# Performance work log

Measured on AMD Instinct MI355X. Metric: run time of the kernel, lower is better.

## Reference

```python
import jax, jax.numpy as jnp
import numpy as np

DIM = 512
HID = 512
H = 8
HD = HID // H
RB_HID = 64
COORD = 3


def setup_inputs() -> dict:
    key = jax.random.key(0)
    ks = jax.random.split(key, 12)
    B, Nq, Nk = 2, 1024, 2048
    s = 0.02
    return {
        "q_in": jax.random.normal(ks[0], (B, Nq, DIM), jnp.float32),
        "kv_in": jax.random.normal(ks[1], (B, Nk, DIM), jnp.float32),
        "q_coords": jax.random.normal(ks[2], (B, Nq, COORD), jnp.float32),
        "kv_coords": jax.random.normal(ks[3], (B, Nk, COORD), jnp.float32),
        "Wq": jax.random.normal(ks[4], (DIM, HID), jnp.float32) * s,
        "Wk": jax.random.normal(ks[5], (DIM, HID), jnp.float32) * s,
        "Wv": jax.random.normal(ks[6], (DIM, HID), jnp.float32) * s,
        "Wo": jax.random.normal(ks[7], (HID, DIM), jnp.float32) * s,
        "W1": jax.random.normal(ks[8], (1, RB_HID), jnp.float32) * s,
        "b1": jnp.zeros((RB_HID,), jnp.float32),
        "W2": jax.random.normal(ks[9], (RB_HID, H), jnp.float32) * s,
        "b2": jnp.zeros((H,), jnp.float32),
    }


def reference(q_in, kv_in, q_coords, kv_coords, Wq, Wk, Wv, Wo, W1, b1, W2, b2):
    B, Nq, _ = q_in.shape
    Nk = kv_in.shape[1]
    # projections -> [B, H, N, HD]
    q = (q_in @ Wq).reshape(B, Nq, H, HD).transpose(0, 2, 1, 3)
    k = (kv_in @ Wk).reshape(B, Nk, H, HD).transpose(0, 2, 1, 3)
    v = (kv_in @ Wv).reshape(B, Nk, H, HD).transpose(0, 2, 1, 3)
    # pairwise Euclidean distance [B, Nq, Nk]
    diff = q_coords[:, :, None, :] - kv_coords[:, None, :, :]
    d = jnp.sqrt(jnp.sum(diff * diff, axis=-1))
    # 2-layer MLP on distance -> per-head bias [B, H, Nq, Nk]
    h = jax.nn.silu(d[..., None] * W1[0] + b1)  # [B,Nq,Nk,RB_HID]
    bias = (h @ W2 + b2).transpose(0, 3, 1, 2)  # [B,H,Nq,Nk]
    scale = HD ** -0.5
    logits = jnp.einsum("bhqd,bhkd->bhqk", q, k) * scale + bias
    attn = jax.nn.softmax(logits, axis=-1)
    out = jnp.einsum("bhqk,bhkd->bhqd", attn, v)
    out = out.transpose(0, 2, 1, 3).reshape(B, Nq, HID)
    return out @ Wo
```

## Files before the change

kernel.cpp:

```cpp
#include <hip/hip_runtime.h>
#include <hip/hip_bf16.h>
#include <math.h>

typedef short bf16x8 __attribute__((ext_vector_type(8)));
typedef float f32x4 __attribute__((ext_vector_type(4)));
typedef unsigned short u16;
typedef unsigned int u32;

#define NH 8
#define BB 2
#define NQ 1024
#define NK 2048
#define NSPLIT 8
#define M2CONST 6.4921250
#define SC2 0.18033688f
#define LS 68

#define MFMA16(a, b, c) __builtin_amdgcn_mfma_f32_16x16x32_bf16(a, b, c, 0, 0, 0)

__device__ __constant__ double XN_D[6] = {251.63850576500074, 218.50966799187810,
                                          161.12883777312265, 94.871162226877350,
                                          37.490330081221910, 4.3614942349992570};

static __device__ __forceinline__ u32 bfr(float x) {
  u32 u = __builtin_bit_cast(u32, x);
  return u + 0x7FFFu + ((u >> 16) & 1u);
}
static __device__ __forceinline__ u32 pk2(float lo, float hi) {
  return (bfr(lo) >> 16) | (bfr(hi) & 0xFFFF0000u);
}
static __device__ __forceinline__ u16 bfs(float x) { return (u16)(bfr(x) >> 16); }

static __device__ __forceinline__ bf16x8 pack8(float4 a, float4 b) {
  union { bf16x8 v; uint4 u; } cv;
  cv.u.x = pk2(a.x, a.y);
  cv.u.y = pk2(a.z, a.w);
  cv.u.z = pk2(b.x, b.y);
  cv.u.w = pk2(b.z, b.w);
  return cv.v;
}

__global__ __launch_bounds__(256) void setup_kernel(
    const float* __restrict__ Wq, const float* __restrict__ Wk,
    const float* __restrict__ Wv, const float* __restrict__ Wo,
    u16* __restrict__ Tq, u16* __restrict__ Tk,
    u16* __restrict__ Tv, u16* __restrict__ To,
    const float* __restrict__ W1, const float* __restrict__ b1,
    const float* __restrict__ W2, const float* __restrict__ b2,
    float* __restrict__ polyc,
    const float* __restrict__ kc, u16* __restrict__ keg) {
  const int blk = blockIdx.x, t = threadIdx.x;
  if (blk < 256) {
    __shared__ u16 tile[64][65];
    const float* W; u16* Wt;
    switch (blk >> 6) {
      case 0: W = Wq; Wt = Tq; break;
      case 1: W = Wk; Wt = Tk; break;
      case 2: W = Wv; Wt = Tv; break;
      default: W = Wo; Wt = To; break;
    }
    const int rem = blk & 63;
    const int k0 = (rem >> 3) * 64, n0 = (rem & 7) * 64;
    const int r = t >> 4, c4 = (t & 15) * 4;
    #pragma unroll
    for (int p = 0; p < 4; p++) {
      int row = p * 16 + r;
      float4 v = *(const float4*)&W[(size_t)(k0 + row) * 512 + n0 + c4];
      tile[row][c4 + 0] = bfs(v.x);
      tile[row][c4 + 1] = bfs(v.y);
      tile[row][c4 + 2] = bfs(v.z);
      tile[row][c4 + 3] = bfs(v.w);
    }
    __syncthreads();
    #pragma unroll
    for (int p = 0; p < 4; p++) {
      int n = p * 16 + r;
      u16 u0 = tile[c4 + 0][n], u1 = tile[c4 + 1][n];
      u16 u2 = tile[c4 + 2][n], u3 = tile[c4 + 3][n];
      uint2 o;
      o.x = u0 | ((u32)u1 << 16);
      o.y = u2 | ((u32)u3 << 16);
      *(uint2*)&Wt[(size_t)(n0 + n) * 512 + k0 + c4] = o;
    }
  } else if (blk == 256) {
    __shared__ double fv[6][8];
    if (t < 48) {
      int i = t >> 3, h = t & 7;
      double x = sqrt(XN_D[i]);
      double acc = (double)b2[h];
      for (int r = 0; r < 64; r++) {
        double u = x * (double)W1[r] + (double)b1[r];
        double s = u / (1.0 + exp(-u));
        acc += s * (double)W2[r * 8 + h];
      }
      fv[i][h] = acc * 1.4426950408889634 - M2CONST;
    }
    __syncthreads();
    if (t < 8) {
      int h = t;
      double c[6];
      #pragma unroll
      for (int i = 0; i < 6; i++) c[i] = fv[i][h];
      for (int k = 1; k < 6; k++)
        for (int i = 5; i >= k; i--)
          c[i] = (c[i] - c[i - 1]) / (XN_D[i] - XN_D[i - k]);
      double m[6] = {c[5], 0, 0, 0, 0, 0};
      int deg = 0;
      for (int i = 4; i >= 0; i--) {
        double np[6] = {};
        for (int j = deg; j >= 0; j--) np[j + 1] += m[j];
        for (int j = 0; j <= deg; j++) np[j] -= XN_D[i] * m[j];
        np[0] += c[i];
        deg++;
        for (int j = 0; j <= deg; j++) m[j] = np[j];
      }
      #pragma unroll
      for (int j = 0; j < 6; j++) polyc[h * 8 + j] = (float)m[j];
    }
  } else {
    int r = (blk - 257) * 256 + t;
    float kx = kc[(size_t)r * 3], ky = kc[(size_t)r * 3 + 1], kz = kc[(size_t)r * 3 + 2];
    uint4 o;
    o.x = pk2(-2.0f * kx, -2.0f * ky);
    o.y = pk2(-2.0f * kz, 1.0f);
    o.z = (u32)bfs(kx * kx + ky * ky + kz * kz);
    o.w = 0;
    *(uint4*)&keg[(size_t)r * 8] = o;
  }
}

__global__ __launch_bounds__(256) void gemm_qkv(
    const float* __restrict__ q_in, const float* __restrict__ kv_in,
    const u16* __restrict__ Wqt, const u16* __restrict__ Wkt,
    const u16* __restrict__ Wvt, u16* __restrict__ Qp,
    u16* __restrict__ Kp, u16* __restrict__ Vtp) {
  __shared__ u16 As[64 * LS];
  __shared__ u16 Bs[64 * LS];
  __shared__ u16 Bs2[64 * LS];
  const int t = threadIdx.x;
  const int w = t >> 6, l = t & 63, g = l >> 4, li = l & 15;
  const int bx = blockIdx.x;
  const bool isQ = bx < 32;
  const int m0 = (isQ ? bx : bx - 32) * 64, n0 = blockIdx.y * 64;
  const float* A = isQ ? q_in : kv_in;
  const u16* B1 = isQ ? Wqt : Wkt;
  const int ms = (w & 1) * 32, ns = (w >> 1) * 32;
  const int ar = t >> 2, ac = (t & 3) * 16;
  f32x4 acc[2][2] = {}, accV[2][2] = {};

  for (int kt = 0; kt < 512; kt += 64) {
    float4 a4[4];
    #pragma unroll
    for (int q = 0; q < 4; q++)
      a4[q] = *(const float4*)&A[(size_t)(m0 + ar) * 512 + kt + ac + 4 * q];
    bf16x8 bk[2], bv2[2];
    #pragma unroll
    for (int p = 0; p < 2; p++) {
      int f = p * 256 + t, r = f >> 3, c8 = (f & 7) * 8;
      bk[p] = *(const bf16x8*)&B1[(size_t)(n0 + r) * 512 + kt + c8];
    }
    if (!isQ) {
      #pragma unroll
      for (int p = 0; p < 2; p++) {
        int f = p * 256 + t, r = f >> 3, c8 = (f & 7) * 8;
        bv2[p] = *(const bf16x8*)&Wvt[(size_t)(n0 + r) * 512 + kt + c8];
      }
    }
    __syncthreads();
    *(bf16x8*)&As[ar * LS + ac] = pack8(a4[0], a4[1]);
    *(bf16x8*)&As[ar * LS + ac + 8] = pack8(a4[2], a4[3]);
    #pragma unroll
    for (int p = 0; p < 2; p++) {
      int f = p * 256 + t, r = f >> 3, c8 = (f & 7) * 8;
      *(bf16x8*)&Bs[r * LS + c8] = bk[p];
    }
    if (!isQ) {
      #pragma unroll
      for (int p = 0; p < 2; p++) {
        int f = p * 256 + t, r = f >> 3, c8 = (f & 7) * 8;
        *(bf16x8*)&Bs2[r * LS + c8] = bv2[p];
      }
    }
    __syncthreads();
    #pragma unroll
    for (int ks = 0; ks < 2; ks++) {
      bf16x8 a0 = *(const bf16x8*)&As[(ms + li) * LS + ks * 32 + g * 8];
      bf16x8 a1 = *(const bf16x8*)&As[(ms + 16 + li) * LS + ks * 32 + g * 8];
      bf16x8 k0 = *(const bf16x8*)&Bs[(ns + li) * LS + ks * 32 + g * 8];
      bf16x8 k1 = *(const bf16x8*)&Bs[(ns + 16 + li) * LS + ks * 32 + g * 8];
      acc[0][0] = MFMA16(a0, k0, acc[0][0]);
      acc[0][1] = MFMA16(a0, k1, acc[0][1]);
      acc[1][0] = MFMA16(a1, k0, acc[1][0]);
      acc[1][1] = MFMA16(a1, k1, acc[1][1]);
      if (!isQ) {
        bf16x8 v0 = *(const bf16x8*)&Bs2[(ns + li) * LS + ks * 32 + g * 8];
        bf16x8 v1 = *(const bf16x8*)&Bs2[(ns + 16 + li) * LS + ks * 32 + g * 8];
        accV[0][0] = MFMA16(a0, v0, accV[0][0]);
        accV[0][1] = MFMA16(a0, v1, accV[0][1]);
        accV[1][0] = MFMA16(a1, v0, accV[1][0]);
        accV[1][1] = MFMA16(a1, v1, accV[1][1]);
      }
    }
  }
  #pragma unroll
  for (int mi = 0; mi < 2; mi++) {
    #pragma unroll
    for (int ni = 0; ni < 2; ni++) {
      int row = m0 + ms + mi * 16 + 4 * g;
      int col = n0 + ns + ni * 16 + li;
      f32x4 vk = acc[mi][ni];
      if (isQ) {
        #pragma unroll
        for (int r = 0; r < 4; r++) Qp[(size_t)(row + r) * 512 + col] = bfs(vk[r]);
      } else {
        #pragma unroll
        for (int r = 0; r < 4; r++) Kp[(size_t)(row + r) * 512 + col] = bfs(vk[r]);
        f32x4 vv = accV[mi][ni];
        int bb = row >> 11, j = row & 2047;
        int hh = col >> 6, d = col & 63;
        uint2 o;
        o.x = pk2(vv[0], vv[1]);
        o.y = pk2(vv[2], vv[3]);
        *(uint2*)&Vtp[((size_t)((bb * 8 + hh) * 64 + d)) * 2048 + j] = o;
      }
    }
  }
}

__global__ __launch_bounds__(256, 4) void attn_kernel(
    const u16* __restrict__ Qb, const u16* __restrict__ Kb,
    const u16* __restrict__ Vt, const float* __restrict__ qc,
    const u16* __restrict__ keg, const float* __restrict__ polyc,
    float* __restrict__ Op, float* __restrict__ Lp) {
  __shared__ u16 Kl[64 * LS];
  __shared__ u16 Vtl[64 * LS];
  __shared__ u16 Pl[64 * LS];

  const int t = threadIdx.x;
  const int w = t >> 6, l = t & 63, g = l >> 4, li = l & 15;
  const int qt = blockIdx.x >> 3, sidx = blockIdx.x & 7;
  const int h = blockIdx.y, b = blockIdx.z;

  const float c0 = polyc[h * 8 + 0], c1 = polyc[h * 8 + 1];
  const float c2 = polyc[h * 8 + 2], c3 = polyc[h * 8 + 3];
  const float c4 = polyc[h * 8 + 4], c5 = polyc[h * 8 + 5];

  const int qrow = qt * 64 + w * 16 + li;
  const size_t qg = (size_t)b * NQ + qrow;
  bf16x8 qf0 = *(const bf16x8*)&Qb[qg * 512 + h * 64 + g * 8];
  bf16x8 qf1 = *(const bf16x8*)&Qb[qg * 512 + h * 64 + 32 + g * 8];
  float qx = qc[qg * 3], qy = qc[qg * 3 + 1], qz = qc[qg * 3 + 2];
  bf16x8 qe = {};
  if (g == 0) {
    qe[0] = (short)bfs(qx);
    qe[1] = (short)bfs(qy);
    qe[2] = (short)bfs(qz);
    qe[3] = (short)bfs(qx * qx + qy * qy + qz * qz);
    qe[4] = (short)bfs(1.0f);
  }

  f32x4 oacc[4] = {};
  float lacc = 0.0f;

  const u16* Kg = Kb + (size_t)b * NK * 512 + h * 64;
  const u16* Vg = Vt + (size_t)((b * 8 + h) * 64) * 2048;
  const u16* keg_b = keg + (size_t)b * NK * 8;

  const int jb0 = sidx * (NK / NSPLIT);
  const int srow = t >> 3, sc8 = (t & 7) * 8;

  bf16x8 kr0 = *(const bf16x8*)&Kg[(size_t)(jb0 + srow) * 512 + sc8];
  bf16x8 kr1 = *(const bf16x8*)&Kg[(size_t)(jb0 + 32 + srow) * 512 + sc8];
  bf16x8 vr0 = *(const bf16x8*)&Vg[(size_t)srow * 2048 + jb0 + sc8];
  bf16x8 vr1 = *(const bf16x8*)&Vg[(size_t)(32 + srow) * 2048 + jb0 + sc8];

  for (int it = 0; it < NK / NSPLIT / 64; it++) {
    const int jbase = jb0 + it * 64;
    __syncthreads();
    *(bf16x8*)&Kl[srow * LS + sc8] = kr0;
    *(bf16x8*)&Kl[(32 + srow) * LS + sc8] = kr1;
    *(bf16x8*)&Vtl[srow * LS + sc8] = vr0;
    *(bf16x8*)&Vtl[(32 + srow) * LS + sc8] = vr1;
    __syncthreads();
    if (it + 1 < NK / NSPLIT / 64) {
      const int jn = jbase + 64;
      kr0 = *(const bf16x8*)&Kg[(size_t)(jn + srow) * 512 + sc8];
      kr1 = *(const bf16x8*)&Kg[(size_t)(jn + 32 + srow) * 512 + sc8];
      vr0 = *(const bf16x8*)&Vg[(size_t)srow * 2048 + jn + sc8];
      vr1 = *(const bf16x8*)&Vg[(size_t)(32 + srow) * 2048 + jn + sc8];
    }

    #pragma unroll
    for (int j4 = 0; j4 < 4; j4++) {
      bf16x8 ka0 = *(const bf16x8*)&Kl[(j4 * 16 + li) * LS + g * 8];
      bf16x8 ka1 = *(const bf16x8*)&Kl[(j4 * 16 + li) * LS + 32 + g * 8];
      f32x4 z = {};
      f32x4 s0 = MFMA16(ka0, qf0, z);
      f32x4 sac = MFMA16(ka1, qf1, s0);
      bf16x8 ke = {};
      if (g == 0)
        ke = *(const bf16x8*)&keg_b[(size_t)(jbase + j4 * 16 + li) * 8];
      f32x4 dac = MFMA16(ke, qe, z);

      float p[4];
      #pragma unroll
      for (int r = 0; r < 4; r++) {
        float u = fminf(dac[r], 256.0f);
        float gp = fmaf(fmaf(fmaf(fmaf(fmaf(c5, u, c4), u, c3), u, c2), u, c1), u, c0);
        p[r] = __builtin_amdgcn_exp2f(fmaf(sac[r], SC2, gp));
      }
      lacc += (p[0] + p[1]) + (p[2] + p[3]);
      uint2 pv;
      pv.x = pk2(p[0], p[1]);
      pv.y = pk2(p[2], p[3]);
      *(uint2*)&Pl[(w * 16 + li) * LS + j4 * 16 + g * 4] = pv;
    }

    bf16x8 pf0 = *(const bf16x8*)&Pl[(w * 16 + li) * LS + g * 8];
    bf16x8 pf1 = *(const bf16x8*)&Pl[(w * 16 + li) * LS + 32 + g * 8];
    #pragma unroll
    for (int dt = 0; dt < 4; dt++) {
      bf16x8 v0 = *(const bf16x8*)&Vtl[(dt * 16 + li) * LS + g * 8];
      bf16x8 v1 = *(const bf16x8*)&Vtl[(dt * 16 + li) * LS + 32 + g * 8];
      oacc[dt] = MFMA16(pf0, v0, oacc[dt]);
      oacc[dt] = MFMA16(pf1, v1, oacc[dt]);
    }
  }

  float lf = lacc;
  lf += __shfl_xor(lf, 16);
  lf += __shfl_xor(lf, 32);

  const size_t obase =
      ((size_t)(sidx * 16 + b * 8 + h) * 1024 + qt * 64 + w * 16) * 64;
  #pragma unroll
  for (int dt = 0; dt < 4; dt++)
    #pragma unroll
    for (int r = 0; r < 4; r++)
      Op[obase + (size_t)(4 * g + r) * 64 + dt * 16 + li] = oacc[dt][r];
  if (g == 0)
    Lp[(size_t)(sidx * 16 + b * 8 + h) * 1024 + qt * 64 + w * 16 + li] = lf;
}

__global__ __launch_bounds__(256) void combine_kernel(const float* __restrict__ Op,
                                                      const float* __restrict__ Lp,
                                                      u16* __restrict__ AOb) {
  int tid = blockIdx.x * 256 + threadIdx.x;
  int d4 = tid & 15, rh = tid >> 4;
  int bh = rh >> 10, qrow = rh & 1023;
  f32x4 o = {};
  float lsum = 0.0f;
  #pragma unroll
  for (int s = 0; s < NSPLIT; s++) {
    f32x4 v = *(const f32x4*)&Op[((size_t)(s * 16 + bh) * 1024 + qrow) * 64 + d4 * 4];
    o += v;
    lsum += Lp[(size_t)(s * 16 + bh) * 1024 + qrow];
  }
  float inv = __builtin_amdgcn_rcpf(lsum);
  uint2 pk;
  pk.x = pk2(o[0] * inv, o[1] * inv);
  pk.y = pk2(o[2] * inv, o[3] * inv);
  *(uint2*)&AOb[((size_t)(bh >> 3) * NQ + qrow) * 512 + (bh & 7) * 64 + d4 * 4] = pk;
}

__global__ __launch_bounds__(256) void gemm_wo(const u16* __restrict__ A,
                                               const u16* __restrict__ Bt,
                                               float* __restrict__ C) {
  __shared__ u16 As[32 * LS];
  __shared__ u16 Bs[64 * LS];
  const int t = threadIdx.x;
  const int w = t >> 6, l = t & 63, g = l >> 4, li = l & 15;
  const int m0 = blockIdx.x * 32, n0 = blockIdx.y * 64;
  const int ms = (w & 1) * 16, ns = (w >> 1) * 32;
  f32x4 acc[2] = {};
  for (int kt = 0; kt < 512; kt += 64) {
    bf16x8 av, bv[2];
    {
      int r = t >> 3, c8 = (t & 7) * 8;
      av = *(const bf16x8*)&A[(size_t)(m0 + r) * 512 + kt + c8];
    }
    #pragma unroll
    for (int p = 0; p < 2; p++) {
      int f = p * 256 + t, r = f >> 3, c8 = (f & 7) * 8;
      bv[p] = *(const bf16x8*)&Bt[(size_t)(n0 + r) * 512 + kt + c8];
    }
    __syncthreads();
    {
      int r = t >> 3, c8 = (t & 7) * 8;
      *(bf16x8*)&As[r * LS + c8] = av;
    }
    #pragma unroll
    for (int p = 0; p < 2; p++) {
      int f = p * 256 + t, r = f >> 3, c8 = (f & 7) * 8;
      *(bf16x8*)&Bs[r * LS + c8] = bv[p];
    }
    __syncthreads();
    #pragma unroll
    for (int ks = 0; ks < 2; ks++) {
      bf16x8 af = *(const bf16x8*)&As[(ms + li) * LS + ks * 32 + g * 8];
      bf16x8 b0 = *(const bf16x8*)&Bs[(ns + li) * LS + ks * 32 + g * 8];
      bf16x8 b1 = *(const bf16x8*)&Bs[(ns + 16 + li) * LS + ks * 32 + g * 8];
      acc[0] = MFMA16(af, b0, acc[0]);
      acc[1] = MFMA16(af, b1, acc[1]);
    }
  }
  #pragma unroll
  for (int ni = 0; ni < 2; ni++) {
    f32x4 v = acc[ni];
    int row = m0 + ms + 4 * g;
    int col = n0 + ns + ni * 16 + li;
    #pragma unroll
    for (int r = 0; r < 4; r++) C[(size_t)(row + r) * 512 + col] = v[r];
  }
}

extern "C" void kernel_launch(void* const* d_in, const int* in_sizes, int n_in,
                              void* d_out, int out_size, void* d_ws, size_t ws_size,
                              hipStream_t stream) {
  const float* q_in      = (const float*)d_in[0];
  const float* kv_in     = (const float*)d_in[1];
  const float* q_coords  = (const float*)d_in[2];
  const float* kv_coords = (const float*)d_in[3];
  const float* Wq        = (const float*)d_in[4];
  const float* Wk        = (const float*)d_in[5];
  const float* Wv        = (const float*)d_in[6];
  const float* Wo        = (const float*)d_in[7];
  const float* W1        = (const float*)d_in[8];
  const float* b1        = (const float*)d_in[9];
  const float* W2        = (const float*)d_in[10];
  const float* b2        = (const float*)d_in[11];

  char* p = (char*)d_ws;
  u16* Wqt  = (u16*)p; p += (size_t)512 * 512 * 2;
  u16* Wkt  = (u16*)p; p += (size_t)512 * 512 * 2;
  u16* Wvt  = (u16*)p; p += (size_t)512 * 512 * 2;
  u16* Wot  = (u16*)p; p += (size_t)512 * 512 * 2;
  u16* Qp   = (u16*)p; p += (size_t)2048 * 512 * 2;
  u16* Kp   = (u16*)p; p += (size_t)4096 * 512 * 2;
  u16* Vtp  = (u16*)p; p += (size_t)4096 * 512 * 2;
  u16* AOb  = (u16*)p; p += (size_t)2048 * 512 * 2;
  u16* keg  = (u16*)p; p += (size_t)4096 * 8 * 2;
  float* polyc = (float*)p; p += (size_t)64 * 4;
  p = (char*)(((size_t)p + 255) & ~(size_t)255);
  float* Opart = (float*)p; p += (size_t)NSPLIT * 16 * 1024 * 64 * 4;
  float* Lpart = (float*)p; p += (size_t)NSPLIT * 16 * 1024 * 4;

  setup_kernel<<<273, 256, 0, stream>>>(Wq, Wk, Wv, Wo, Wqt, Wkt, Wvt, Wot,
                                        W1, b1, W2, b2, polyc, kv_coords, keg);
  gemm_qkv<<<dim3(96, 8), 256, 0, stream>>>(q_in, kv_in, Wqt, Wkt, Wvt,
                                            Qp, Kp, Vtp);
  attn_kernel<<<dim3(128, 8, 2), 256, 0, stream>>>(Qp, Kp, Vtp, q_coords, keg,
                                                   polyc, Opart, Lpart);
  combine_kernel<<<1024, 256, 0, stream>>>(Opart, Lpart, AOb);
  gemm_wo<<<dim3(64, 8), 256, 0, stream>>>(AOb, Wot, (float*)d_out);
}
```

Baseline: 147.5 us.

## Pre-convert activations to bf16 in setup and fuse split-K combine into attention

The setup kernel gains extra blocks that convert q_in and kv_in to bf16 once, so the QKV GEMM loads bf16 tiles directly instead of re-reading and converting fp32 activations in every N-tile block. The separate combine kernel is removed; each attention block bumps an atomic counter per (bh, q-tile), and the last of the eight splits reduces the partial outputs and writes the bf16 attention output. This saves a kernel launch and redundant fp32 reads of the activations. In exchange it adds an extra bf16 write/read pass, threadfence and atomic overhead, and a serialized tail on the last-arriving block.

```diff
diff --git a/kernel.cpp b/kernel.cpp
--- a/kernel.cpp
+++ b/kernel.cpp
@@ -31,15 +31,6 @@
 }
 static __device__ __forceinline__ u16 bfs(float x) { return (u16)(bfr(x) >> 16); }
 
-static __device__ __forceinline__ bf16x8 pack8(float4 a, float4 b) {
-  union { bf16x8 v; uint4 u; } cv;
-  cv.u.x = pk2(a.x, a.y);
-  cv.u.y = pk2(a.z, a.w);
-  cv.u.z = pk2(b.x, b.y);
-  cv.u.w = pk2(b.z, b.w);
-  return cv.v;
-}
-
 __global__ __launch_bounds__(256) void setup_kernel(
     const float* __restrict__ Wq, const float* __restrict__ Wk,
     const float* __restrict__ Wv, const float* __restrict__ Wo,
@@ -48,9 +39,22 @@
     const float* __restrict__ W1, const float* __restrict__ b1,
     const float* __restrict__ W2, const float* __restrict__ b2,
     float* __restrict__ polyc,
-    const float* __restrict__ kc, u16* __restrict__ keg) {
+    const float* __restrict__ kc, u16* __restrict__ keg,
+    const float* __restrict__ q_in, const float* __restrict__ kv_in,
+    u16* __restrict__ qb, u16* __restrict__ kvb, int* __restrict__ cnt) {
   const int blk = blockIdx.x, t = threadIdx.x;
-  if (blk < 256) {
+  if (blk >= 273 && blk < 1809) {
+    int gi = (blk - 273) * 256 + t;
+    const float* src; u16* dst; size_t off;
+    if (gi < 131072) { src = q_in; dst = qb; off = (size_t)gi * 8; }
+    else             { src = kv_in; dst = kvb; off = (size_t)(gi - 131072) * 8; }
+    float4 a = *(const float4*)(src + off);
+    float4 b = *(const float4*)(src + off + 4);
+    uint4 o;
+    o.x = pk2(a.x, a.y); o.y = pk2(a.z, a.w);
+    o.z = pk2(b.x, b.y); o.w = pk2(b.z, b.w);
+    *(uint4*)(dst + off) = o;
+  } else if (blk < 256) {
     __shared__ u16 tile[64][65];
     const float* W; u16* Wt;
     switch (blk >> 6) {
@@ -117,7 +121,7 @@
       #pragma unroll
       for (int j = 0; j < 6; j++) polyc[h * 8 + j] = (float)m[j];
     }
-  } else {
+  } else if (blk < 273) {
     int r = (blk - 257) * 256 + t;
     float kx = kc[(size_t)r * 3], ky = kc[(size_t)r * 3 + 1], kz = kc[(size_t)r * 3 + 2];
     uint4 o;
@@ -126,11 +130,13 @@
     o.z = (u32)bfs(kx * kx + ky * ky + kz * kz);
     o.w = 0;
     *(uint4*)&keg[(size_t)r * 8] = o;
+  } else {
+    cnt[t] = 0;
   }
 }
 
 __global__ __launch_bounds__(256) void gemm_qkv(
-    const float* __restrict__ q_in, const float* __restrict__ kv_in,
+    const u16* __restrict__ qb, const u16* __restrict__ kvb,
     const u16* __restrict__ Wqt, const u16* __restrict__ Wkt,
     const u16* __restrict__ Wvt, u16* __restrict__ Qp,
     u16* __restrict__ Kp, u16* __restrict__ Vtp) {
@@ -142,21 +148,17 @@
   const int bx = blockIdx.x;
   const bool isQ = bx < 32;
   const int m0 = (isQ ? bx : bx - 32) * 64, n0 = blockIdx.y * 64;
-  const float* A = isQ ? q_in : kv_in;
+  const u16* A = isQ ? qb : kvb;
   const u16* B1 = isQ ? Wqt : Wkt;
   const int ms = (w & 1) * 32, ns = (w >> 1) * 32;
-  const int ar = t >> 2, ac = (t & 3) * 16;
   f32x4 acc[2][2] = {}, accV[2][2] = {};
 
   for (int kt = 0; kt < 512; kt += 64) {
-    float4 a4[4];
-    #pragma unroll
-    for (int q = 0; q < 4; q++)
-      a4[q] = *(const float4*)&A[(size_t)(m0 + ar) * 512 + kt + ac + 4 * q];
-    bf16x8 bk[2], bv2[2];
+    bf16x8 av[2], bk[2], bv2[2];
     #pragma unroll
     for (int p = 0; p < 2; p++) {
       int f = p * 256 + t, r = f >> 3, c8 = (f & 7) * 8;
+      av[p] = *(const bf16x8*)&A[(size_t)(m0 + r) * 512 + kt + c8];
       bk[p] = *(const bf16x8*)&B1[(size_t)(n0 + r) * 512 + kt + c8];
     }
     if (!isQ) {
@@ -167,11 +169,10 @@
       }
     }
     __syncthreads();
-    *(bf16x8*)&As[ar * LS + ac] = pack8(a4[0], a4[1]);
-    *(bf16x8*)&As[ar * LS + ac + 8] = pack8(a4[2], a4[3]);
     #pragma unroll
     for (int p = 0; p < 2; p++) {
       int f = p * 256 + t, r = f >> 3, c8 = (f & 7) * 8;
+      *(bf16x8*)&As[r * LS + c8] = av[p];
       *(bf16x8*)&Bs[r * LS + c8] = bk[p];
     }
     if (!isQ) {
@@ -231,15 +232,18 @@
     const u16* __restrict__ Qb, const u16* __restrict__ Kb,
     const u16* __restrict__ Vt, const float* __restrict__ qc,
     const u16* __restrict__ keg, const float* __restrict__ polyc,
-    float* __restrict__ Op, float* __restrict__ Lp) {
+    float* __restrict__ Op, float* __restrict__ Lp,
+    int* __restrict__ cnt, u16* __restrict__ AOb) {
   __shared__ u16 Kl[64 * LS];
   __shared__ u16 Vtl[64 * LS];
   __shared__ u16 Pl[64 * LS];
+  __shared__ int lastflag;
 
   const int t = threadIdx.x;
   const int w = t >> 6, l = t & 63, g = l >> 4, li = l & 15;
   const int qt = blockIdx.x >> 3, sidx = blockIdx.x & 7;
   const int h = blockIdx.y, b = blockIdx.z;
+  const int bh = b * 8 + h;
 
   const float c0 = polyc[h * 8 + 0], c1 = polyc[h * 8 + 1];
   const float c2 = polyc[h * 8 + 2], c3 = polyc[h * 8 + 3];
@@ -332,35 +336,48 @@
   lf += __shfl_xor(lf, 32);
 
   const size_t obase =
-      ((size_t)(sidx * 16 + b * 8 + h) * 1024 + qt * 64 + w * 16) * 64;
+      ((size_t)(sidx * 16 + bh) * 1024 + qt * 64 + w * 16) * 64;
   #pragma unroll
   for (int dt = 0; dt < 4; dt++)
     #pragma unroll
     for (int r = 0; r < 4; r++)
       Op[obase + (size_t)(4 * g + r) * 64 + dt * 16 + li] = oacc[dt][r];
   if (g == 0)
-    Lp[(size_t)(sidx * 16 + b * 8 + h) * 1024 + qt * 64 + w * 16 + li] = lf;
-}
-
-__global__ __launch_bounds__(256) void combine_kernel(const float* __restrict__ Op,
-                                                      const float* __restrict__ Lp,
-                                                      u16* __restrict__ AOb) {
-  int tid = blockIdx.x * 256 + threadIdx.x;
-  int d4 = tid & 15, rh = tid >> 4;
-  int bh = rh >> 10, qrow = rh & 1023;
-  f32x4 o = {};
-  float lsum = 0.0f;
-  #pragma unroll
-  for (int s = 0; s < NSPLIT; s++) {
-    f32x4 v = *(const f32x4*)&Op[((size_t)(s * 16 + bh) * 1024 + qrow) * 64 + d4 * 4];
-    o += v;
-    lsum += Lp[(size_t)(s * 16 + bh) * 1024 + qrow];
-  }
-  float inv = __builtin_amdgcn_rcpf(lsum);
-  uint2 pk;
-  pk.x = pk2(o[0] * inv, o[1] * inv);
-  pk.y = pk2(o[2] * inv, o[3] * inv);
-  *(uint2*)&AOb[((size_t)(bh >> 3) * NQ + qrow) * 512 + (bh & 7) * 64 + d4 * 4] = pk;
+    Lp[(size_t)(sidx * 16 + bh) * 1024 + qt * 64 + w * 16 + li] = lf;
+
+  __threadfence();
+  if (t == 0)
+    lastflag = (atomicAdd(&cnt[bh * 16 + qt], 1) == NSPLIT - 1);
+  __syncthreads();
+  if (lastflag) {
+    __threadfence();
+    const int row = t >> 2, d0 = (t & 3) * 16;
+    f32x4 s0 = {}, s1 = {}, s2 = {}, s3 = {};
+    float lsum = 0.0f;
+    #pragma unroll
+    for (int s = 0; s < NSPLIT; s++) {
+      const float* base =
+          &Op[((size_t)(s * 16 + bh) * 1024 + qt * 64 + row) * 64 + d0];
+      s0 += *(const f32x4*)(base + 0);
+      s1 += *(const f32x4*)(base + 4);
+      s2 += *(const f32x4*)(base + 8);
+      s3 += *(const f32x4*)(base + 12);
+      lsum += Lp[(size_t)(s * 16 + bh) * 1024 + qt * 64 + row];
+    }
+    float inv = __builtin_amdgcn_rcpf(lsum);
+    uint4 o0, o1;
+    o0.x = pk2(s0[0] * inv, s0[1] * inv);
+    o0.y = pk2(s0[2] * inv, s0[3] * inv);
+    o0.z = pk2(s1[0] * inv, s1[1] * inv);
+    o0.w = pk2(s1[2] * inv, s1[3] * inv);
+    o1.x = pk2(s2[0] * inv, s2[1] * inv);
+    o1.y = pk2(s2[2] * inv, s2[3] * inv);
+    o1.z = pk2(s3[0] * inv, s3[1] * inv);
+    o1.w = pk2(s3[2] * inv, s3[3] * inv);
+    u16* dst = &AOb[((size_t)b * NQ + qt * 64 + row) * 512 + h * 64 + d0];
+    *(uint4*)dst = o0;
+    *(uint4*)(dst + 8) = o1;
+  }
 }
 
 __global__ __launch_bounds__(256) void gemm_wo(const u16* __restrict__ A,
@@ -435,22 +452,25 @@
   u16* Wkt  = (u16*)p; p += (size_t)512 * 512 * 2;
   u16* Wvt  = (u16*)p; p += (size_t)512 * 512 * 2;
   u16* Wot  = (u16*)p; p += (size_t)512 * 512 * 2;
+  u16* qb   = (u16*)p; p += (size_t)2048 * 512 * 2;
+  u16* kvb  = (u16*)p; p += (size_t)4096 * 512 * 2;
   u16* Qp   = (u16*)p; p += (size_t)2048 * 512 * 2;
   u16* Kp   = (u16*)p; p += (size_t)4096 * 512 * 2;
   u16* Vtp  = (u16*)p; p += (size_t)4096 * 512 * 2;
   u16* AOb  = (u16*)p; p += (size_t)2048 * 512 * 2;
   u16* keg  = (u16*)p; p += (size_t)4096 * 8 * 2;
   float* polyc = (float*)p; p += (size_t)64 * 4;
+  int* cnt  = (int*)p; p += (size_t)256 * 4;
   p = (char*)(((size_t)p + 255) & ~(size_t)255);
   float* Opart = (float*)p; p += (size_t)NSPLIT * 16 * 1024 * 64 * 4;
   float* Lpart = (float*)p; p += (size_t)NSPLIT * 16 * 1024 * 4;
 
-  setup_kernel<<<273, 256, 0, stream>>>(Wq, Wk, Wv, Wo, Wqt, Wkt, Wvt, Wot,
-                                        W1, b1, W2, b2, polyc, kv_coords, keg);
-  gemm_qkv<<<dim3(96, 8), 256, 0, stream>>>(q_in, kv_in, Wqt, Wkt, Wvt,
+  setup_kernel<<<1810, 256, 0, stream>>>(Wq, Wk, Wv, Wo, Wqt, Wkt, Wvt, Wot,
+                                         W1, b1, W2, b2, polyc, kv_coords, keg,
+                                         q_in, kv_in, qb, kvb, cnt);
+  gemm_qkv<<<dim3(96, 8), 256, 0, stream>>>(qb, kvb, Wqt, Wkt, Wvt,
                                             Qp, Kp, Vtp);
   attn_kernel<<<dim3(128, 8, 2), 256, 0, stream>>>(Qp, Kp, Vtp, q_coords, keg,
-                                                   polyc, Opart, Lpart);
-  combine_kernel<<<1024, 256, 0, stream>>>(Opart, Lpart, AOb);
+                                                   polyc, Opart, Lpart, cnt, AOb);
   gemm_wo<<<dim3(64, 8), 256, 0, stream>>>(AOb, Wot, (float*)d_out);
 }
```

Result: slower. 569.8 us (+286.2%).
